# Kernel optimization log

Measured on AMD Instinct MI355X. Metric: run time of the kernel, lower is better.

The kernel has to match this reference:

```python
import jax, jax.numpy as jnp
import numpy as np

NG, SNG, NS, SNS, NR = 4, 2, 4, 2, 3
NW = 4
STEP = 1 + NG + SNG + NS + SNS + NR  # 16
T, D = 512, 64
MARGIN, ALPHA, BETA, P, R = 1.0, 0.01, 1.0, 0.1, 0.1
KNUM, KMUL = 5, 2.0
GAMMA = 5.0          # soft-dtw gamma
BIG = 1e9            # finite 'inf' so softmin grads stay NaN-free
SIZ = NW * (NW + 1) // 2  # mmds buffer size in the original (zero padded)


def setup_inputs() -> dict:
    key = jax.random.key(0)
    k1, k2 = jax.random.split(key)
    data = jax.random.normal(k1, (NW * STEP, T, D), dtype=jnp.float32)
    lens = jax.random.randint(k2, (NW * STEP,), 64, T + 1, dtype=jnp.int32)
    return {"data": data, "lens": lens}


def _softdtw(Dmat, la, lb):
    """Soft-DTW via anti-diagonal scan. Dmat: (T,T) squared-euclid costs.
    Returns R[la, lb]; DP cells only depend on smaller indices so padding is inert."""
    Tn = Dmat.shape[0]
    idx = jnp.arange(Tn)

    def step(carry, k):
        r2, r1 = carry                      # diagonals k-2 and k-1, indexed by i
        j = k - idx
        valid = (j >= 0) & (j < Tn)
        d = jnp.where(valid, Dmat[idx, jnp.clip(j, 0, Tn - 1)], BIG)
        up = jnp.where(idx > 0, jnp.roll(r1, 1), BIG)     # cell (i-1, j)
        left = r1                                          # cell (i, j-1)
        diag = jnp.where(idx > 0, jnp.roll(r2, 1), BIG)    # cell (i-1, j-1)
        diag = jnp.where((idx == 0) & (k == 0), 0.0, diag)  # R[0,0] = 0 border
        m = jnp.stack([diag, up, left])
        softmin = -GAMMA * jax.nn.logsumexp(-m / GAMMA, axis=0)
        r = jnp.where(valid, d + softmin, BIG)
        return (r1, r), r

    init = (jnp.full((Tn,), BIG, Dmat.dtype), jnp.full((Tn,), BIG, Dmat.dtype))
    _, rows = jax.lax.scan(step, init, jnp.arange(2 * Tn - 1))
    # rows[k, i] = R[i+1, k-i+1]; want R[la, lb] -> k = la+lb-2, i = la-1
    return rows[la + lb - 2, la - 1]


def _mmd(x, y):
    """Multi-kernel Gaussian MMD (DAN-style MMDLoss), n == m."""
    n = x.shape[0]
    total = jnp.concatenate([x, y], axis=0)          # (2n, F)
    sq = jnp.sum(total * total, axis=1)
    l2 = sq[:, None] + sq[None, :] - 2.0 * (total @ total.T)
    ns = total.shape[0]
    bw = jnp.sum(l2) / (ns * ns - ns)
    bw = bw / (KMUL ** (KNUM // 2))
    bws = bw * (KMUL ** jnp.arange(KNUM, dtype=total.dtype))
    kern = jnp.sum(jnp.exp(-l2[None] / bws[:, None, None]), axis=0)
    XX, YY, XY, YX = kern[:n, :n], kern[n:, n:], kern[:n, n:], kern[n:, :n]
    return jnp.mean(XX + YY - XY - YX)


def _forward(data, lens):
    d = data.reshape(NW, STEP, T, D)
    li = lens.reshape(NW, STEP)
    Lf = li.astype(data.dtype)
    anchors = d[:, 0]          # (nw, T, D)
    others = d[:, 1:]          # (nw, 15, T, D)

    # squared-euclidean cost matrices via GEMM: (nw, 15, T, T)
    a2 = jnp.sum(anchors * anchors, -1)                      # (nw, T)
    b2 = jnp.sum(others * others, -1)                        # (nw, 15, T)
    ab = jnp.einsum('wtd,wjsd->wjts', anchors, others)
    cost = a2[:, None, :, None] + b2[:, :, None, :] - 2.0 * ab

    laB = jnp.broadcast_to(li[:, :1], (NW, STEP - 1))
    sdt = jax.vmap(jax.vmap(_softdtw))(cost, laB, li[:, 1:])  # (nw, 15)
    dist = sdt / (Lf[:, :1] + Lf[:, 1:])

    dist_g = dist[:, :NG + SNG]    # genuine + synthetic genuine (6)
    dist_n = dist[:, NG + SNG:]    # skilled + syn skilled + random (9)

    lk = jax.nn.relu(dist_g[:, :, None] + MARGIN - dist_n[:, None, :])
    ca = jnp.mean(dist_g, axis=1)
    cb = jnp.mean(dist_n[:, :5], axis=1)
    intra = jnp.sum(dist_g - ca[:, None], axis=1)
    inter = jax.nn.relu(BETA - jnp.abs(ca - cb))
    nz = jnp.sum(lk != 0, axis=(1, 2))
    lv = jnp.sum(lk, axis=(1, 2)) / (nz + 1).astype(data.dtype)
    total_loss = jnp.mean(lv + intra * P + inter * R)

    # MMD over all (i, j) pairs written by the original loop (i in 0..nw-1,
    # j in 1..nw-1, i != j); buffer zero-padded to SIZ, then max * alpha.
    groups = d[:, :STEP - 5].reshape(NW, STEP - 5, T * D)
    pi = jnp.array([0, 0, 0, 1, 1, 2, 2, 3, 3])
    pj = jnp.array([1, 2, 3, 2, 3, 1, 3, 1, 2])
    mmds = jax.vmap(_mmd)(groups[pi], groups[pj])
    mmds = jnp.concatenate([mmds, jnp.zeros((SIZ - pi.shape[0],), data.dtype)])
    mmd1 = jnp.max(mmds) * ALPHA
    return total_loss + mmd1


def reference(data, lens):
    return _forward(data, lens)
```

## Files before the change

kernel.cpp:

```cpp
#include <hip/hip_runtime.h>
#include <hip/hip_fp16.h>

#define TT   512
#define DD   64
#define NWK  4
#define STP  16
#define NPJ  15
#define NBLK 60
#define CMAT (TT * TT)
#define CSCALE 0.2885390081777927f
#define USCALE 3.4657359027997265f
#define BIGC   2.885390081777927e8f

#define SA 132
#define SMEMSZ (2 * DD * SA * 4 + 1024)

__device__ __forceinline__ float dpcell(float dc, float a, float b, float c) {
  float mn = fminf(fminf(a, b), c);
  float mx = fmaxf(fmaxf(a, b), c);
  float md = __builtin_amdgcn_fmed3f(a, b, c);
  float e = 1.0f + __builtin_amdgcn_exp2f(mn - md) + __builtin_amdgcn_exp2f(mn - mx);
  return dc + mn - __builtin_amdgcn_logf(e);
}

__device__ __forceinline__ float wave_shr1(float x) {
  int xi = __float_as_int(x);
  int r = __builtin_amdgcn_update_dpp(xi, xi, 0x138 , 0xF, 0xF, false);
  return __int_as_float(r);
}

__global__ __launch_bounds__(64) void zero_kernel(int* __restrict__ cnt) {
  cnt[threadIdx.x] = 0;
}

__global__ __launch_bounds__(256) void mega_kernel(const float* __restrict__ data,
                                                   const int* __restrict__ lens,
                                                   __half* __restrict__ cost,
                                                   float* __restrict__ sdt,
                                                   float* __restrict__ gram,
                                                   int* __restrict__ cnt,
                                                   int base, int n, int ng) {
  __shared__ __align__(16) char smem[SMEMSZ];
  int b = blockIdx.x;

  if (b >= n + ng) {
    int cb = b - n - ng;
    int mloc = cb >> 4, tile = cb & 15;
    int blk = base + mloc;
    int w = blk / NPJ, j = blk - w * NPJ;
    int la = lens[w * STP];
    int lb = lens[w * STP + 1 + j];
    int ti = tile >> 2, tj = tile & 3;
    if (ti * 128 >= la || tj * 128 >= lb) {
      if (threadIdx.x == 0) atomicAdd(&cnt[mloc], 1);
      return;
    }

    float (*As)[SA] = (float(*)[SA])smem;
    float (*Bs)[SA] = (float(*)[SA])(smem + DD * SA * 4);
    float* a2 = (float*)(smem + 2 * DD * SA * 4);
    float* b2 = a2 + 128;

    const float* A = data + ((size_t)(w * STP) * TT + (size_t)ti * 128) * DD;
    const float* B = data + ((size_t)(w * STP + 1 + j) * TT + (size_t)tj * 128) * DD;
    int t = threadIdx.x;

    #pragma unroll
    for (int i = 0; i < 8; ++i) {
      int idx = t + i * 256;
      int r = idx & 127;
      int kq = idx >> 7;
      float4 va = *(const float4*)(A + r * DD + kq * 4);
      As[kq * 4 + 0][r] = va.x; As[kq * 4 + 1][r] = va.y;
      As[kq * 4 + 2][r] = va.z; As[kq * 4 + 3][r] = va.w;
      float4 vb = *(const float4*)(B + r * DD + kq * 4);
      Bs[kq * 4 + 0][r] = vb.x; Bs[kq * 4 + 1][r] = vb.y;
      Bs[kq * 4 + 2][r] = vb.z; Bs[kq * 4 + 3][r] = vb.w;
    }
    __syncthreads();
    if (t < 128) {
      float s = 0.f;
      for (int k = 0; k < DD; ++k) { float x = As[k][t]; s += x * x; }
      a2[t] = s;
    } else {
      float s = 0.f;
      for (int k = 0; k < DD; ++k) { float x = Bs[k][t - 128]; s += x * x; }
      b2[t - 128] = s;
    }
    __syncthreads();

    int r0 = (t >> 4) << 2;
    int c0 = (t & 15) << 2;
    float acc[8][8];
    #pragma unroll
    for (int i = 0; i < 8; ++i)
      #pragma unroll
      for (int q = 0; q < 8; ++q) acc[i][q] = 0.f;

    #pragma unroll 2
    for (int k = 0; k < DD; ++k) {
      float4 aL = *(const float4*)&As[k][r0];
      float4 aH = *(const float4*)&As[k][r0 + 64];
      float4 bL = *(const float4*)&Bs[k][c0];
      float4 bH = *(const float4*)&Bs[k][c0 + 64];
      float a[8] = {aL.x, aL.y, aL.z, aL.w, aH.x, aH.y, aH.z, aH.w};
      float bq[8] = {bL.x, bL.y, bL.z, bL.w, bH.x, bH.y, bH.z, bH.w};
      #pragma unroll
      for (int i = 0; i < 8; ++i)
        #pragma unroll
        for (int q = 0; q < 8; ++q)
          acc[i][q] += a[i] * bq[q];
    }

    __half* Cbase = cost + (size_t)mloc * CMAT;
    #pragma unroll
    for (int i = 0; i < 8; ++i) {
      int rr = (i < 4) ? (r0 + i) : (r0 + 60 + i);
      float ar = a2[rr];
      __half* Crow = Cbase + (size_t)(ti * 128 + rr) * TT + tj * 128;
      float4 o;
      o.x = (ar + b2[c0 + 0] - 2.f * acc[i][0]) * CSCALE;
      o.y = (ar + b2[c0 + 1] - 2.f * acc[i][1]) * CSCALE;
      o.z = (ar + b2[c0 + 2] - 2.f * acc[i][2]) * CSCALE;
      o.w = (ar + b2[c0 + 3] - 2.f * acc[i][3]) * CSCALE;
      __half2 h01 = __floats2half2_rn(o.x, o.y);
      __half2 h23 = __floats2half2_rn(o.z, o.w);
      uint2 pk; pk.x = *(unsigned*)&h01; pk.y = *(unsigned*)&h23;
      *(uint2*)(Crow + c0) = pk;
      float4 o2;
      o2.x = (ar + b2[c0 + 64] - 2.f * acc[i][4]) * CSCALE;
      o2.y = (ar + b2[c0 + 65] - 2.f * acc[i][5]) * CSCALE;
      o2.z = (ar + b2[c0 + 66] - 2.f * acc[i][6]) * CSCALE;
      o2.w = (ar + b2[c0 + 67] - 2.f * acc[i][7]) * CSCALE;
      __half2 g01 = __floats2half2_rn(o2.x, o2.y);
      __half2 g23 = __floats2half2_rn(o2.z, o2.w);
      uint2 pk2; pk2.x = *(unsigned*)&g01; pk2.y = *(unsigned*)&g23;
      *(uint2*)(Crow + c0 + 64) = pk2;
    }
    __syncthreads();
    if (threadIdx.x == 0) {
      __threadfence();
      atomicAdd(&cnt[mloc], 1);
    }
    return;
  }

  if (b >= n) {
    float (*red)[16] = (float(*)[16])smem;
    int g = b - n;
    int bx = g / 11, by = g - bx * 11;
    int t = threadIdx.x;
    const float* Ar[4]; const float* Br[4];
    #pragma unroll
    for (int a = 0; a < 4; ++a) {
      int gx = bx * 4 + a;
      Ar[a] = data + (size_t)((gx / 11) * STP + gx % 11) * (TT * DD);
      int gy = by * 4 + a;
      Br[a] = data + (size_t)((gy / 11) * STP + gy % 11) * (TT * DD);
    }
    float acc[4][4];
    #pragma unroll
    for (int a = 0; a < 4; ++a)
      #pragma unroll
      for (int bq = 0; bq < 4; ++bq) acc[a][bq] = 0.f;
    for (int k = t * 4; k < TT * DD; k += 1024) {
      float4 av[4], bv[4];
      #pragma unroll
      for (int a = 0; a < 4; ++a) av[a] = *(const float4*)(Ar[a] + k);
      #pragma unroll
      for (int bq = 0; bq < 4; ++bq) bv[bq] = *(const float4*)(Br[bq] + k);
      #pragma unroll
      for (int a = 0; a < 4; ++a)
        #pragma unroll
        for (int bq = 0; bq < 4; ++bq)
          acc[a][bq] += av[a].x * bv[bq].x + av[a].y * bv[bq].y +
                        av[a].z * bv[bq].z + av[a].w * bv[bq].w;
    }
    int wave = t >> 6, lane = t & 63;
    #pragma unroll
    for (int a = 0; a < 4; ++a)
      #pragma unroll
      for (int bq = 0; bq < 4; ++bq) {
        float v = acc[a][bq];
        for (int off = 32; off > 0; off >>= 1) v += __shfl_down(v, off);
        if (lane == 0) red[wave][a * 4 + bq] = v;
      }
    __syncthreads();
    if (t < 16) {
      float v = red[0][t] + red[1][t] + red[2][t] + red[3][t];
      int a = t >> 2, bq = t & 3;
      gram[(size_t)(bx * 4 + a) * 44 + by * 4 + bq] = v;
    }
    return;
  }

  int mloc = b;
  if (threadIdx.x == 0) {
    while (__hip_atomic_load(&cnt[mloc], __ATOMIC_ACQUIRE, __HIP_MEMORY_SCOPE_AGENT) < 16)
      __builtin_amdgcn_s_sleep(2);
  }
  __syncthreads();
  __threadfence();

  float (*bufB)[600] = (float(*)[600])smem;
  int* flags = (int*)(smem + 3 * 600 * 4);

  if (threadIdx.x < 4) flags[threadIdx.x] = 0;
  __syncthreads();

  int blk = base + mloc;
  int w = blk / NPJ, j = blk - w * NPJ;
  int la = lens[w * STP];
  int lb = lens[w * STP + 1 + j];
  const __half* C = cost + (size_t)mloc * CMAT;

  int q = threadIdx.x >> 6, ln = threadIdx.x & 63;
  int c0 = q * 128 + ln * 2;
  const __half* Cp = C + c0;

  int qt = (lb - 1) >> 7;
  int lt = ((lb - 1) >> 1) & 63;
  int par = (lb - 1) & 1;
  int rt = la - 1;
  bool isT = (q == qt) && (ln == lt);

  float U0 = BIGC, U1 = BIGC;
  float NL = BIGC;
  float NLd = (q == 0 && ln == 0) ? 0.0f : BIGC;
  float v1s = BIGC;
  float res = 0.0f;

  int ngrp = (la + 70) >> 3;

  float2 cc[8];
  unsigned cn[8];
  #pragma unroll
  for (int k = 0; k < 8; ++k) {
    int rr = k - ln; rr = rr < 0 ? 0 : (rr > 511 ? 511 : rr);
    __half2 hv = *(const __half2*)(Cp + (size_t)rr * TT);
    cc[k] = __half22float2(hv);
  }
  float bb[8];

  for (int g = 0; g < ngrp; ++g) {
    if (q > 0) {
      int need = 8 * g + 9; if (need > la) need = la;
      while (*(volatile int*)&flags[q - 1] < need) __builtin_amdgcn_s_sleep(1);
      asm volatile("s_waitcnt lgkmcnt(0)" ::: "memory");
      #pragma unroll
      for (int k = 0; k < 8; ++k) bb[k] = bufB[q - 1][8 * g + 1 + k];
      if (g == 0) {
        float nl0 = bufB[q - 1][0];
        if (ln == 0) NL = nl0;
      }
    }
    #pragma unroll
    for (int k = 0; k < 8; ++k) {
      int rr = 8 * (g + 1) + k - ln; rr = rr < 0 ? 0 : (rr > 511 ? 511 : rr);
      cn[k] = *(const unsigned*)(Cp + (size_t)rr * TT);
    }
    #pragma unroll
    for (int k = 0; k < 8; ++k) {
      int r = 8 * g + k - ln;
      bool act = ((unsigned)r < 512u);
      if (act) {
        float v0 = dpcell(cc[k].x, NLd, U0, NL);
        float v1 = dpcell(cc[k].y, U0, U1, v0);
        if (isT & (r == rt)) res = par ? v1 : v0;
        NLd = NL; U0 = v0; U1 = v1; v1s = v1;
        if (q < 3 && ln == 63) {
          bufB[q][r] = v1;
          if ((r & 7) == 0) {
            asm volatile("s_waitcnt lgkmcnt(0)" ::: "memory");
            *(volatile int*)&flags[q] = r + 1;
          }
        }
      }
      float nb = wave_shr1(v1s);
      if (ln == 0) nb = (q == 0) ? BIGC : bb[k];
      NL = nb;
    }
    #pragma unroll
    for (int k = 0; k < 8; ++k) {
      __half2 hv = *(__half2*)&cn[k];
      cc[k] = __half22float2(hv);
    }
  }
  if (q < 3 && ln == 63) {
    asm volatile("s_waitcnt lgkmcnt(0)" ::: "memory");
    *(volatile int*)&flags[q] = 512;
  }
  if (isT) sdt[blk] = res * USCALE;
}

__global__ __launch_bounds__(640) void final_kernel(const float* __restrict__ sdt,
                                                    const int* __restrict__ lens,
                                                    const float* __restrict__ gram,
                                                    float* __restrict__ out) {
  __shared__ float partial[16];
  int t = threadIdx.x, wave = t >> 6, lane = t & 63;
  if (wave < 9) {
    const int piA[9] = {0, 0, 0, 1, 1, 2, 2, 3, 3};
    const int pjA[9] = {1, 2, 3, 2, 3, 1, 3, 1, 2};
    int P = piA[wave], Q = pjA[wave];
    float s1 = 0.f;
    for (int c = lane; c < 484; c += 64) {
      int i = c / 22, jj = c - (c / 22) * 22;
      int gi = (i < 11) ? P * 11 + i : Q * 11 + (i - 11);
      int gj = (jj < 11) ? P * 11 + jj : Q * 11 + (jj - 11);
      s1 += gram[gi * 44 + gi] + gram[gj * 44 + gj] - 2.f * gram[gi * 44 + gj];
    }
    for (int off = 32; off > 0; off >>= 1) s1 += __shfl_down(s1, off);
    s1 = __shfl(s1, 0);
    float bw = s1 / 462.0f * 0.25f;
    float inv[5];
    float b = bw;
    #pragma unroll
    for (int qq = 0; qq < 5; ++qq) { inv[qq] = -1.0f / b; b *= 2.0f; }
    float s2 = 0.f;
    for (int c = lane; c < 484; c += 64) {
      int i = c / 22, jj = c - (c / 22) * 22;
      int gi = (i < 11) ? P * 11 + i : Q * 11 + (i - 11);
      int gj = (jj < 11) ? P * 11 + jj : Q * 11 + (jj - 11);
      float l2 = gram[gi * 44 + gi] + gram[gj * 44 + gj] - 2.f * gram[gi * 44 + gj];
      float kk = 0.f;
      #pragma unroll
      for (int qq = 0; qq < 5; ++qq) kk += __expf(l2 * inv[qq]);
      float sgn = ((i < 11) == (jj < 11)) ? 1.0f : -1.0f;
      s2 += sgn * kk;
    }
    for (int off = 32; off > 0; off >>= 1) s2 += __shfl_down(s2, off);
    if (lane == 0) partial[wave] = s2 / 121.0f;
  } else {
    float term = 0.f;
    if (wave == 9 && lane < 4) {
      int w = lane;
      float L0 = (float)lens[w * STP];
      float dist[15];
      for (int qq = 0; qq < 15; ++qq)
        dist[qq] = sdt[w * NPJ + qq] / (L0 + (float)lens[w * STP + 1 + qq]);
      float ca = 0.f, cb = 0.f;
      for (int a = 0; a < 6; ++a) ca += dist[a];
      ca *= (1.0f / 6.0f);
      for (int bq = 6; bq < 11; ++bq) cb += dist[bq];
      cb *= (1.0f / 5.0f);
      float lksum = 0.f; int nz = 0;
      for (int a = 0; a < 6; ++a)
        for (int bq = 6; bq < 15; ++bq) {
          float x = dist[a] + 1.0f - dist[bq];
          if (x > 0.f) { lksum += x; nz += 1; }
        }
      float intra = 0.f;
      for (int a = 0; a < 6; ++a) intra += dist[a] - ca;
      float inter = fmaxf(0.f, 1.0f - fabsf(ca - cb));
      term = lksum / (float)(nz + 1) + intra * 0.1f + inter * 0.1f;
    }
    if (wave == 9) {
      term += __shfl_down(term, 1);
      term += __shfl_down(term, 2);
      if (lane == 0) partial[9] = term * 0.25f;
    }
  }
  __syncthreads();
  if (t == 0) {
    float mx = 0.0f;
    for (int p = 0; p < 9; ++p) mx = fmaxf(mx, partial[p]);
    out[0] = partial[9] + 0.01f * mx;
  }
}

extern "C" void kernel_launch(void* const* d_in, const int* in_sizes, int n_in,
                              void* d_out, int out_size, void* d_ws, size_t ws_size,
                              hipStream_t stream) {
  const float* data = (const float*)d_in[0];
  const int* lens = (const int*)d_in[1];
  float* out = (float*)d_out;

  float* sdtb  = (float*)d_ws;
  float* gramb = sdtb + 64;
  int*   cntb  = (int*)((char*)d_ws + 8192);
  __half* costh = (__half*)((char*)d_ws + 8448);

  size_t avail = (ws_size > 8448) ? (ws_size - 8448) : 0;
  int chunk = (int)(avail / ((size_t)CMAT * sizeof(__half)));
  if (chunk < 1) chunk = 1;
  if (chunk > NBLK) chunk = NBLK;

  bool first = true;
  for (int base = 0; base < NBLK; base += chunk) {
    int n = NBLK - base;
    if (n > chunk) n = chunk;
    int ng = first ? 121 : 0;
    zero_kernel<<<1, 64, 0, stream>>>(cntb);
    mega_kernel<<<n + ng + 16 * n, 256, 0, stream>>>(data, lens, costh, sdtb, gramb,
                                                     cntb, base, n, ng);
    first = false;
  }
  final_kernel<<<1, 640, 0, stream>>>(sdtb, lens, gramb, out);
}
```

Before: 245.2 us.

## Stage cost-tile operands in fp16 shared memory and launch tile blocks before gram blocks

The cost-matrix tile blocks now convert inputs to half precision when staging them in shared memory. This halves LDS footprint, which may raise occupancy of the whole mega kernel, and halves LDS read traffic in the inner product loop. Block ordering is also rearranged so cost-tile blocks are dispatched right after the DP blocks and ahead of the MMD gram blocks, getting the tiles the DP consumers wait on started sooner. The fp16 rounding of inputs changes distance precision and adds conversion instructions in the inner loop.

```diff
diff --git a/kernel.cpp b/kernel.cpp
--- a/kernel.cpp
+++ b/kernel.cpp
@@ -13,7 +13,7 @@
 #define BIGC   2.885390081777927e8f
 
 #define SA 132
-#define SMEMSZ (2 * DD * SA * 4 + 1024)
+#define SMEMSZ (2 * DD * SA * 2 + 1024)
 
 __device__ __forceinline__ float dpcell(float dc, float a, float b, float c) {
   float mn = fminf(fminf(a, b), c);
@@ -43,8 +43,8 @@
   __shared__ __align__(16) char smem[SMEMSZ];
   int b = blockIdx.x;
 
-  if (b >= n + ng) {
-    int cb = b - n - ng;
+  if (b >= n && b < n + 16 * n) {
+    int cb = b - n;
     int mloc = cb >> 4, tile = cb & 15;
     int blk = base + mloc;
     int w = blk / NPJ, j = blk - w * NPJ;
@@ -56,9 +56,9 @@
       return;
     }
 
-    float (*As)[SA] = (float(*)[SA])smem;
-    float (*Bs)[SA] = (float(*)[SA])(smem + DD * SA * 4);
-    float* a2 = (float*)(smem + 2 * DD * SA * 4);
+    __half (*As)[SA] = (__half(*)[SA])smem;
+    __half (*Bs)[SA] = (__half(*)[SA])(smem + DD * SA * 2);
+    float* a2 = (float*)(smem + 2 * DD * SA * 2);
     float* b2 = a2 + 128;
 
     const float* A = data + ((size_t)(w * STP) * TT + (size_t)ti * 128) * DD;
@@ -71,20 +71,20 @@
       int r = idx & 127;
       int kq = idx >> 7;
       float4 va = *(const float4*)(A + r * DD + kq * 4);
-      As[kq * 4 + 0][r] = va.x; As[kq * 4 + 1][r] = va.y;
-      As[kq * 4 + 2][r] = va.z; As[kq * 4 + 3][r] = va.w;
+      As[kq * 4 + 0][r] = __float2half(va.x); As[kq * 4 + 1][r] = __float2half(va.y);
+      As[kq * 4 + 2][r] = __float2half(va.z); As[kq * 4 + 3][r] = __float2half(va.w);
       float4 vb = *(const float4*)(B + r * DD + kq * 4);
-      Bs[kq * 4 + 0][r] = vb.x; Bs[kq * 4 + 1][r] = vb.y;
-      Bs[kq * 4 + 2][r] = vb.z; Bs[kq * 4 + 3][r] = vb.w;
+      Bs[kq * 4 + 0][r] = __float2half(vb.x); Bs[kq * 4 + 1][r] = __float2half(vb.y);
+      Bs[kq * 4 + 2][r] = __float2half(vb.z); Bs[kq * 4 + 3][r] = __float2half(vb.w);
     }
     __syncthreads();
     if (t < 128) {
       float s = 0.f;
-      for (int k = 0; k < DD; ++k) { float x = As[k][t]; s += x * x; }
+      for (int k = 0; k < DD; ++k) { float x = __half2float(As[k][t]); s += x * x; }
       a2[t] = s;
     } else {
       float s = 0.f;
-      for (int k = 0; k < DD; ++k) { float x = Bs[k][t - 128]; s += x * x; }
+      for (int k = 0; k < DD; ++k) { float x = __half2float(Bs[k][t - 128]); s += x * x; }
       b2[t - 128] = s;
     }
     __syncthreads();
@@ -99,12 +99,16 @@
 
     #pragma unroll 2
     for (int k = 0; k < DD; ++k) {
-      float4 aL = *(const float4*)&As[k][r0];
-      float4 aH = *(const float4*)&As[k][r0 + 64];
-      float4 bL = *(const float4*)&Bs[k][c0];
-      float4 bH = *(const float4*)&Bs[k][c0 + 64];
-      float a[8] = {aL.x, aL.y, aL.z, aL.w, aH.x, aH.y, aH.z, aH.w};
-      float bq[8] = {bL.x, bL.y, bL.z, bL.w, bH.x, bH.y, bH.z, bH.w};
+      const __half2* pAL = (const __half2*)&As[k][r0];
+      const __half2* pAH = (const __half2*)&As[k][r0 + 64];
+      const __half2* pBL = (const __half2*)&Bs[k][c0];
+      const __half2* pBH = (const __half2*)&Bs[k][c0 + 64];
+      float2 a0 = __half22float2(pAL[0]), a1 = __half22float2(pAL[1]);
+      float2 a2v = __half22float2(pAH[0]), a3 = __half22float2(pAH[1]);
+      float2 b0 = __half22float2(pBL[0]), b1 = __half22float2(pBL[1]);
+      float2 b2v = __half22float2(pBH[0]), b3 = __half22float2(pBH[1]);
+      float a[8] = {a0.x, a0.y, a1.x, a1.y, a2v.x, a2v.y, a3.x, a3.y};
+      float bq[8] = {b0.x, b0.y, b1.x, b1.y, b2v.x, b2v.y, b3.x, b3.y};
       #pragma unroll
       for (int i = 0; i < 8; ++i)
         #pragma unroll
@@ -145,9 +149,9 @@
     return;
   }
 
-  if (b >= n) {
+  if (b >= n + 16 * n) {
     float (*red)[16] = (float(*)[16])smem;
-    int g = b - n;
+    int g = b - n - 16 * n;
     int bx = g / 11, by = g - bx * 11;
     int t = threadIdx.x;
     const float* Ar[4]; const float* Br[4];
@@ -392,7 +396,7 @@
     if (n > chunk) n = chunk;
     int ng = first ? 121 : 0;
     zero_kernel<<<1, 64, 0, stream>>>(cntb);
-    mega_kernel<<<n + ng + 16 * n, 256, 0, stream>>>(data, lens, costh, sdtb, gramb,
+    mega_kernel<<<n + 16 * n + ng, 256, 0, stream>>>(data, lens, costh, sdtb, gramb,
                                                      cntb, base, n, ng);
     first = false;
   }
```

Result: faster. 239.5 us (-2.3%).
